# Kernel tuning notes

Hardware: AMD Instinct MI355X
Metric: run time of the kernel (lower is better)

## Reference

```python
import jax, jax.numpy as jnp
import numpy as np

V, ENC, D, E = 10000, 2048, 512, 512
B, L = 128, 64


def setup_inputs() -> dict:
    key = jax.random.key(0)
    ks = jax.random.split(key, 12)
    s = lambda *sh: 1.0 / np.sqrt(sh[-1])
    return {
        "global_feats": jax.random.normal(ks[0], (B, ENC), jnp.float32),
        "encoded_captions": jax.random.randint(ks[1], (B, L), 0, V, jnp.int64),
        "caption_lengths": jax.random.randint(ks[2], (B,), 1, L, jnp.int64),
        "W_embed": jax.random.normal(ks[3], (V, E), jnp.float32) * 0.02,
        "W_init": jax.random.normal(ks[4], (D, ENC), jnp.float32) * s(ENC),
        "b_init": jnp.zeros((D,), jnp.float32),
        "W_ih": jax.random.normal(ks[5], (3 * D, E), jnp.float32) * s(E),
        "W_hh": jax.random.normal(ks[6], (3 * D, D), jnp.float32) * s(D),
        "b_ih": jnp.zeros((3 * D,), jnp.float32),
        "b_hh": jnp.zeros((3 * D,), jnp.float32),
        "W_fc": jax.random.normal(ks[7], (V, D), jnp.float32) * s(D),
        "b_fc": jnp.zeros((V,), jnp.float32),
    }


def reference(global_feats, encoded_captions, caption_lengths,
              W_embed, W_init, b_init, W_ih, W_hh, b_ih, b_hh, W_fc, b_fc):
    # init_hidden: h0 = tanh(Linear(global_feats))  -> (B, D)
    h0 = jnp.tanh(global_feats @ W_init.T + b_init)

    # teacher forcing over timesteps 0..L-2 (PyTorch GRU gate order: r, z, n)
    emb = W_embed[encoded_captions[:, : L - 1]]          # (B, L-1, E)
    gi = jnp.einsum('ble,ge->blg', emb, W_ih) + b_ih     # (B, L-1, 3D) precomputed input gates
    gi = jnp.swapaxes(gi, 0, 1)                          # (L-1, B, 3D) scan over time

    def step(h, gi_t):
        gh = h @ W_hh.T + b_hh                           # (B, 3D)
        i_r, i_z, i_n = jnp.split(gi_t, 3, axis=-1)
        h_r, h_z, h_n = jnp.split(gh, 3, axis=-1)
        r = jax.nn.sigmoid(i_r + h_r)
        z = jax.nn.sigmoid(i_z + h_z)
        n = jnp.tanh(i_n + r * h_n)
        h_new = (1.0 - z) * n + z * h
        return h_new, h_new

    _, hs = jax.lax.scan(step, h0, gi)                   # hs: (L-1, B, D)
    # dropout is identity in eval/reference mode
    logits = jnp.einsum('lbd,vd->blv', hs, W_fc) + b_fc  # (B, L-1, V)
    return logits, caption_lengths - 1
```

## Files before the change

### kernel.cpp

```cpp
#include <hip/hip_runtime.h>
#include <hip/hip_bf16.h>

#define V_    10000
#define ENC_  2048
#define D_    512
#define B_    128
#define L_    64
#define T_    63
#define M_    (B_ * L_ - B_)
#define G_    (3 * D_)
#define LOGITS_SZ ((long)M_ * V_)
#define SCAN_NB 64

typedef __bf16 bf16x8_t __attribute__((ext_vector_type(8)));
typedef float  f32x4_t  __attribute__((ext_vector_type(4)));
typedef short  s16x8_t  __attribute__((ext_vector_type(8)));

typedef __attribute__((address_space(3))) char*       lds_cptr_t;
typedef const __attribute__((address_space(1))) char* glb_cptr_t;

__device__ __forceinline__ void gload_lds16(const void* g, void* l) {
  __builtin_amdgcn_global_load_lds((glb_cptr_t)g, (lds_cptr_t)l, 16, 0, 0);
}
__device__ __forceinline__ float bf2f(short s) {
  return __uint_as_float(((unsigned)(unsigned short)s) << 16);
}
__device__ __forceinline__ short f2bf(float f) {
  __hip_bfloat16 h = __float2bfloat16(f);
  return *reinterpret_cast<short*>(&h);
}
__device__ __forceinline__ s16x8_t cvt8(const float* p) {
  f32x4_t lo = *reinterpret_cast<const f32x4_t*>(p);
  f32x4_t hi = *reinterpret_cast<const f32x4_t*>(p + 4);
  s16x8_t r;
#pragma unroll
  for (int e = 0; e < 4; e++) { r[e] = f2bf(lo[e]); r[4 + e] = f2bf(hi[e]); }
  return r;
}
__device__ __forceinline__ float sigmoidf_(float x) {
  return 1.0f / (1.0f + __expf(-x));
}
__device__ __forceinline__ bf16x8_t lds_frag(const short* p) {
  return __builtin_bit_cast(bf16x8_t, *reinterpret_cast<const s16x8_t*>(p));
}

__global__ void GG_cvt_kernel(const float* __restrict__ src,
                              __hip_bfloat16* __restrict__ dst, int n8) {
  int i = blockIdx.x * blockDim.x + threadIdx.x;
  if (i < n8) {
    s16x8_t v = cvt8(src + (long)i * 8);
    *reinterpret_cast<s16x8_t*>(dst + (long)i * 8) = v;
  }
}

__global__ __launch_bounds__(256) void GG_gemm_h0(
    const __hip_bfloat16* __restrict__ gfB,
    const __hip_bfloat16* __restrict__ WinitB,
    const float* __restrict__ binit,
    __hip_bfloat16* __restrict__ hfull) {
  __shared__ short sA[128 * 64];
  __shared__ short sB[128 * 64];
  const int lane = threadIdx.x & 63;
  const int wave = threadIdx.x >> 6;
  const int n0 = blockIdx.x * 128;
  const int srow = lane >> 3;
  const int scol = (lane & 7) * 8;

  f32x4_t acc[4][4] = {};

  const __hip_bfloat16* aptr[4];
  const __hip_bfloat16* bptr[4];
#pragma unroll
  for (int i = 0; i < 4; i++) {
    const int r = (wave * 4 + i) * 8 + srow;
    aptr[i] = gfB + (long)r * ENC_ + scol;
    bptr[i] = WinitB + (long)(n0 + r) * ENC_ + scol;
  }

  const int wm = (wave >> 1) * 64;
  const int wn = (wave & 1) * 64;
  const int fr = lane & 15;
  const int fk = (lane >> 4) * 8;

  for (int kt = 0; kt < 32; kt++) {
    __syncthreads();
#pragma unroll
    for (int i = 0; i < 4; i++) {
      const int chunk = wave * 4 + i;
      gload_lds16(aptr[i] + kt * 64, sA + chunk * 512);
      gload_lds16(bptr[i] + kt * 64, sB + chunk * 512);
    }
    __syncthreads();
#pragma unroll
    for (int kk = 0; kk < 2; kk++) {
      bf16x8_t a[4], b[4];
#pragma unroll
      for (int i = 0; i < 4; i++) {
        a[i] = lds_frag(sA + (wm + i * 16 + fr) * 64 + kk * 32 + fk);
        b[i] = lds_frag(sB + (wn + i * 16 + fr) * 64 + kk * 32 + fk);
      }
#pragma unroll
      for (int i = 0; i < 4; i++)
#pragma unroll
        for (int j = 0; j < 4; j++)
          acc[i][j] = __builtin_amdgcn_mfma_f32_16x16x32_bf16(a[i], b[j], acc[i][j], 0, 0, 0);
    }
  }

  const int fq = lane >> 4;
#pragma unroll
  for (int j = 0; j < 4; j++) {
    const int n = n0 + wn + j * 16 + fr;
    const float bv = binit[n];
#pragma unroll
    for (int i = 0; i < 4; i++)
#pragma unroll
      for (int rr = 0; rr < 4; rr++) {
        const int m = wm + i * 16 + fq * 4 + rr;
        hfull[(long)m * 64 * 512 + n] = __float2bfloat16(tanhf(acc[i][j][rr] + bv));
      }
  }
}

__global__ __launch_bounds__(256) void GG_gemm_gi(
    const __hip_bfloat16* __restrict__ WembB,
    const int* __restrict__ cap,
    const __hip_bfloat16* __restrict__ WihB,
    const float* __restrict__ bias,
    __hip_bfloat16* __restrict__ C) {
  __shared__ short sA[128 * 64];
  __shared__ short sB[128 * 64];
  const int lane = threadIdx.x & 63;
  const int wave = threadIdx.x >> 6;
  const int m0 = blockIdx.y * 128;
  const int n0 = blockIdx.x * 128;
  const int srow = lane >> 3;
  const int scol = (lane & 7) * 8;

  f32x4_t acc[4][4] = {};

  const __hip_bfloat16* aptr[4];
  const __hip_bfloat16* bptr[4];
#pragma unroll
  for (int i = 0; i < 4; i++) {
    const int r = (wave * 4 + i) * 8 + srow;
    const int bt = m0 + r;
    const int bb = bt / 63;
    const int tt = bt - bb * 63;
    aptr[i] = WembB + (long)cap[bb * L_ + tt] * 512 + scol;
    bptr[i] = WihB + (long)(n0 + r) * 512 + scol;
  }

  const int wm = (wave >> 1) * 64;
  const int wn = (wave & 1) * 64;
  const int fr = lane & 15;
  const int fk = (lane >> 4) * 8;

  for (int kt = 0; kt < 8; kt++) {
    __syncthreads();
#pragma unroll
    for (int i = 0; i < 4; i++) {
      const int chunk = wave * 4 + i;
      gload_lds16(aptr[i] + kt * 64, sA + chunk * 512);
      gload_lds16(bptr[i] + kt * 64, sB + chunk * 512);
    }
    __syncthreads();
#pragma unroll
    for (int kk = 0; kk < 2; kk++) {
      bf16x8_t a[4], b[4];
#pragma unroll
      for (int i = 0; i < 4; i++) {
        a[i] = lds_frag(sA + (wm + i * 16 + fr) * 64 + kk * 32 + fk);
        b[i] = lds_frag(sB + (wn + i * 16 + fr) * 64 + kk * 32 + fk);
      }
#pragma unroll
      for (int i = 0; i < 4; i++)
#pragma unroll
        for (int j = 0; j < 4; j++)
          acc[i][j] = __builtin_amdgcn_mfma_f32_16x16x32_bf16(a[i], b[j], acc[i][j], 0, 0, 0);
    }
  }

  const int fq = lane >> 4;
#pragma unroll
  for (int j = 0; j < 4; j++) {
    const int n = n0 + wn + j * 16 + fr;
    const float bv = bias[n];
#pragma unroll
    for (int i = 0; i < 4; i++)
#pragma unroll
      for (int rr = 0; rr < 4; rr++) {
        const int m = m0 + wm + i * 16 + fq * 4 + rr;
        C[(long)m * G_ + n] = __float2bfloat16(acc[i][j][rr] + bv);
      }
  }
}

template <bool BBF16>
__global__ __launch_bounds__(256) void GG_gemm_logits(
    const __hip_bfloat16* __restrict__ hfull,
    const void* __restrict__ Bsrc,
    const float* __restrict__ bias,
    float* __restrict__ C) {
  const int flat = blockIdx.x;
  const int xcd = flat & 7;
  const int s = flat >> 3;
  const int col = xcd * 10 + s % 10;
  const int row = s / 10;
  if (col >= 79) return;
  const int m0 = row * 128;
  const int n0 = col * 128;

  __shared__ short sA[128 * 64];
  __shared__ short sB[128 * 64];
  const int lane = threadIdx.x & 63;
  const int wave = threadIdx.x >> 6;
  const int srow = lane >> 3;
  const int scol = (lane & 7) * 8;

  f32x4_t acc[4][4] = {};

  const __hip_bfloat16* aptr[4];
  const __hip_bfloat16* bptrB[4];
  const float* bptrF[4];
#pragma unroll
  for (int i = 0; i < 4; i++) {
    const int r = (wave * 4 + i) * 8 + srow;
    const int m = m0 + r;
    const int bb = m / 63;
    const int tt = m - bb * 63;
    aptr[i] = hfull + ((long)bb * 64 + tt + 1) * 512 + scol;
    int nrow = n0 + r;
    nrow = (nrow < V_) ? nrow : (V_ - 1);
    if constexpr (BBF16) bptrB[i] = (const __hip_bfloat16*)Bsrc + (long)nrow * 512 + scol;
    else                 bptrF[i] = (const float*)Bsrc + (long)nrow * 512 + scol;
  }

  const int wm = (wave >> 1) * 64;
  const int wn = (wave & 1) * 64;
  const int fr = lane & 15;
  const int fk = (lane >> 4) * 8;

  for (int kt = 0; kt < 8; kt++) {
    s16x8_t vb[4];
    if constexpr (!BBF16) {
#pragma unroll
      for (int i = 0; i < 4; i++) vb[i] = cvt8(bptrF[i] + kt * 64);
    }
    __syncthreads();
#pragma unroll
    for (int i = 0; i < 4; i++) {
      const int chunk = wave * 4 + i;
      gload_lds16(aptr[i] + kt * 64, sA + chunk * 512);
      if constexpr (BBF16)
        gload_lds16(bptrB[i] + kt * 64, sB + chunk * 512);
      else
        *reinterpret_cast<s16x8_t*>(sB + chunk * 512 + lane * 8) = vb[i];
    }
    __syncthreads();
#pragma unroll
    for (int kk = 0; kk < 2; kk++) {
      bf16x8_t a[4], b[4];
#pragma unroll
      for (int i = 0; i < 4; i++) {
        a[i] = lds_frag(sA + (wm + i * 16 + fr) * 64 + kk * 32 + fk);
        b[i] = lds_frag(sB + (wn + i * 16 + fr) * 64 + kk * 32 + fk);
      }
#pragma unroll
      for (int i = 0; i < 4; i++)
#pragma unroll
        for (int j = 0; j < 4; j++)
          acc[i][j] = __builtin_amdgcn_mfma_f32_16x16x32_bf16(a[i], b[j], acc[i][j], 0, 0, 0);
    }
  }

  const int fq = lane >> 4;
#pragma unroll
  for (int j = 0; j < 4; j++) {
    const int n = n0 + wn + j * 16 + fr;
    if (n >= V_) continue;
    const float bv = bias[n];
#pragma unroll
    for (int i = 0; i < 4; i++)
#pragma unroll
      for (int rr = 0; rr < 4; rr++) {
        const int m = m0 + wm + i * 16 + fq * 4 + rr;
        C[(long)m * V_ + n] = acc[i][j][rr] + bv;
      }
  }
}

__global__ __launch_bounds__(256) void GG_scan_persist(
    __hip_bfloat16* __restrict__ hfull,
    const __hip_bfloat16* __restrict__ gi,
    const __hip_bfloat16* __restrict__ WhhB,
    const float* __restrict__ bhh,
    int* __restrict__ ctr) {
  __shared__ short sW[48 * 512];
  __shared__ short sA[4][16 * 512];
  const int lane = threadIdx.x & 63;
  const int wave = threadIdx.x >> 6;
  const int strip = blockIdx.x & 31;
  const int half  = blockIdx.x >> 5;
  const int d0 = strip * 16;
  const int fr = lane & 15;
  const int g4 = lane >> 4;
  int* myctr = ctr + half * 32;

  for (int rr = wave; rr < 48; rr += 4) {
    const int grow = (rr >> 4) * 512 + d0 + (rr & 15);
    gload_lds16(WhhB + (long)grow * 512 + (lane ^ (rr & 7)) * 8, sW + rr * 512);
  }

  const int dd = d0 + fr;
  const int bbase = half * 64 + wave * 16 + g4 * 4;
  const float br_ = bhh[dd], bz_ = bhh[512 + dd], bn_ = bhh[1024 + dd];
  const short* gis = (const short*)gi;
  short* sAw = &sA[wave][0];

  float hp[4];
#pragma unroll
  for (int rr = 0; rr < 4; rr++)
    hp[rr] = bf2f(*(const short*)&hfull[((long)(bbase + rr) * 64) * 512 + dd]);

  asm volatile("s_waitcnt vmcnt(0)" ::: "memory");
  __syncthreads();

  for (int t = 0; t < T_; t++) {
    short gir[4], giz[4], gin[4];
#pragma unroll
    for (int rr = 0; rr < 4; rr++) {
      const long gbase = ((long)(bbase + rr) * T_ + t) * (long)G_;
      gir[rr] = gis[gbase + dd];
      giz[rr] = gis[gbase + 512 + dd];
      gin[rr] = gis[gbase + 1024 + dd];
    }

    if (t > 0) {
      if (threadIdx.x == 0) {
        while (__hip_atomic_load(myctr, __ATOMIC_ACQUIRE, __HIP_MEMORY_SCOPE_AGENT) <
               t * 32)
          __builtin_amdgcn_s_sleep(1);
      }
      __syncthreads();
    }

#pragma unroll
    for (int r = 0; r < 16; r++) {
      const int b = half * 64 + wave * 16 + r;
      gload_lds16(hfull + ((long)b * 64 + t) * 512 + (lane ^ (r & 7)) * 8,
                  sAw + r * 512);
    }
    asm volatile("s_waitcnt vmcnt(0)" ::: "memory");
    __builtin_amdgcn_sched_barrier(0);

    f32x4_t acc[3] = {};
#pragma unroll
    for (int kt = 0; kt < 8; kt++)
#pragma unroll
      for (int kk = 0; kk < 2; kk++) {
        const int kg = kt * 8 + kk * 4 + g4;
        const int gsw = (kg ^ (fr & 7)) * 8;
        bf16x8_t afr = lds_frag(sAw + fr * 512 + gsw);
        bf16x8_t bfr[3];
#pragma unroll
        for (int j = 0; j < 3; j++) bfr[j] = lds_frag(sW + (j * 16 + fr) * 512 + gsw);
#pragma unroll
        for (int j = 0; j < 3; j++)
          acc[j] = __builtin_amdgcn_mfma_f32_16x16x32_bf16(afr, bfr[j], acc[j], 0, 0, 0);
      }

#pragma unroll
    for (int rr = 0; rr < 4; rr++) {
      const float rg = sigmoidf_(bf2f(gir[rr]) + acc[0][rr] + br_);
      const float zg = sigmoidf_(bf2f(giz[rr]) + acc[1][rr] + bz_);
      const float ng = tanhf(bf2f(gin[rr]) + rg * (acc[2][rr] + bn_));
      const short hnb = f2bf((1.f - zg) * ng + zg * hp[rr]);
      hp[rr] = bf2f(hnb);
      *(short*)&hfull[((long)(bbase + rr) * 64 + t + 1) * 512 + dd] = hnb;
    }

    if (t < T_ - 1) {
      __syncthreads();
      if (threadIdx.x == 0)
        __hip_atomic_fetch_add(myctr, 1, __ATOMIC_RELEASE, __HIP_MEMORY_SCOPE_AGENT);
    }
  }
}

__global__ void GG_tail_kernel(const int* __restrict__ lens, float* __restrict__ out) {
  const int b = threadIdx.x;
  if (b < B_) out[LOGITS_SZ + b] = (float)(lens[b] - 1);
}

extern "C" void kernel_launch(void* const* d_in, const int* in_sizes, int n_in,
                              void* d_out, int out_size, void* d_ws, size_t ws_size,
                              hipStream_t stream) {
  const float* gf      = (const float*)d_in[0];
  const int*   cap     = (const int*)d_in[1];
  const int*   lens    = (const int*)d_in[2];
  const float* W_embed = (const float*)d_in[3];
  const float* W_init  = (const float*)d_in[4];
  const float* b_init  = (const float*)d_in[5];
  const float* W_ih    = (const float*)d_in[6];
  const float* W_hh    = (const float*)d_in[7];
  const float* b_ih    = (const float*)d_in[8];
  const float* b_hh    = (const float*)d_in[9];
  const float* W_fc    = (const float*)d_in[10];
  const float* b_fc    = (const float*)d_in[11];
  float* out = (float*)d_out;

  char* ob = (char*)d_out;
  __hip_bfloat16* gi_ws  = (__hip_bfloat16*)ob;
  __hip_bfloat16* WhhB   = (__hip_bfloat16*)(ob + 25165824);
  __hip_bfloat16* WihB   = (__hip_bfloat16*)(ob + 27262976);
  __hip_bfloat16* WembB  = (__hip_bfloat16*)(ob + 29360128);
  __hip_bfloat16* WinitB = (__hip_bfloat16*)(ob + 40894464);
  __hip_bfloat16* gfB    = (__hip_bfloat16*)(ob + 43253760);

  __hip_bfloat16* hfull = (__hip_bfloat16*)d_ws;
  __hip_bfloat16* WfcB  = (__hip_bfloat16*)((char*)d_ws + 8388608);
  const bool big_ws = ws_size >= (size_t)(8388608 + 10240000 + 256);
  int* ctr = (int*)((char*)d_ws + (big_ws ? 18628608 : 8388608));

  hipMemsetAsync(ctr, 0, 256, stream);

  GG_cvt_kernel<<<dim3((G_ * D_ / 8 + 255) / 256), 256, 0, stream>>>(W_hh, WhhB, G_ * D_ / 8);
  GG_cvt_kernel<<<dim3((G_ * D_ / 8 + 255) / 256), 256, 0, stream>>>(W_ih, WihB, G_ * D_ / 8);
  GG_cvt_kernel<<<dim3((V_ * D_ / 8 + 255) / 256), 256, 0, stream>>>(W_embed, WembB, V_ * D_ / 8);
  GG_cvt_kernel<<<dim3((D_ * ENC_ / 8 + 255) / 256), 256, 0, stream>>>(W_init, WinitB, D_ * ENC_ / 8);
  GG_cvt_kernel<<<dim3((B_ * ENC_ / 8 + 255) / 256), 256, 0, stream>>>(gf, gfB, B_ * ENC_ / 8);
  if (big_ws)
    GG_cvt_kernel<<<dim3((V_ * D_ / 8 + 255) / 256), 256, 0, stream>>>(W_fc, WfcB, V_ * D_ / 8);

  GG_gemm_h0<<<dim3(4), 256, 0, stream>>>(gfB, WinitB, b_init, hfull);

  GG_gemm_gi<<<dim3(G_ / 128, M_ / 128), 256, 0, stream>>>(WembB, cap, WihB, b_ih, gi_ws);

  GG_scan_persist<<<dim3(SCAN_NB), 256, 0, stream>>>(hfull, gi_ws, WhhB, b_hh, ctr);

  if (big_ws)
    GG_gemm_logits<true><<<dim3(5040), 256, 0, stream>>>(hfull, WfcB, b_fc, out);
  else
    GG_gemm_logits<false><<<dim3(5040), 256, 0, stream>>>(hfull, W_fc, b_fc, out);

  GG_tail_kernel<<<dim3(1), 128, 0, stream>>>(lens, out);
}
```

Before: 613.6 us.

## Replace scan atomic counter with per-block flags and fuse weight conversions

The persistent GRU scan now signals step completion by having each block store its step number into its own flag, instead of incrementing a shared atomic counter. Waiters poll all 32 flags at once with one wave and a wave vote. Separately, five fp32-to-bf16 conversion launches are merged into one kernel that picks its source by global index. The goal is to cut contention on the single counter and to remove launch overhead, at the cost of a wider polling read and a hard-coded index partition.

Measured after the change: 590.0 us. -3.8%, faster.

```diff
diff --git a/kernel.cpp b/kernel.cpp
--- a/kernel.cpp
+++ b/kernel.cpp
@@ -42,6 +42,22 @@
 }
 __device__ __forceinline__ bf16x8_t lds_frag(const short* p) {
   return __builtin_bit_cast(bf16x8_t, *reinterpret_cast<const s16x8_t*>(p));
+}
+
+__global__ void GG_cvt5(const float* __restrict__ whh, __hip_bfloat16* __restrict__ dwhh,
+                        const float* __restrict__ wih, __hip_bfloat16* __restrict__ dwih,
+                        const float* __restrict__ wemb, __hip_bfloat16* __restrict__ dwemb,
+                        const float* __restrict__ winit, __hip_bfloat16* __restrict__ dwinit,
+                        const float* __restrict__ gf, __hip_bfloat16* __restrict__ dgf) {
+  const int i = blockIdx.x * blockDim.x + threadIdx.x;
+  const float* s; __hip_bfloat16* d; int off;
+  if (i < 98304)        { s = whh;   d = dwhh;   off = i; }
+  else if (i < 196608)  { s = wih;   d = dwih;   off = i - 98304; }
+  else if (i < 836608)  { s = wemb;  d = dwemb;  off = i - 196608; }
+  else if (i < 967680)  { s = winit; d = dwinit; off = i - 836608; }
+  else                  { s = gf;    d = dgf;    off = i - 967680; }
+  s16x8_t v = cvt8(s + (long)off * 8);
+  *reinterpret_cast<s16x8_t*>(d + (long)off * 8) = v;
 }
 
 __global__ void GG_cvt_kernel(const float* __restrict__ src,
@@ -295,7 +311,7 @@
     const __hip_bfloat16* __restrict__ gi,
     const __hip_bfloat16* __restrict__ WhhB,
     const float* __restrict__ bhh,
-    int* __restrict__ ctr) {
+    int* __restrict__ flagbase) {
   __shared__ short sW[48 * 512];
   __shared__ short sA[4][16 * 512];
   const int lane = threadIdx.x & 63;
@@ -305,7 +321,7 @@
   const int d0 = strip * 16;
   const int fr = lane & 15;
   const int g4 = lane >> 4;
-  int* myctr = ctr + half * 32;
+  int* myflags = flagbase + half * 32;
 
   for (int rr = wave; rr < 48; rr += 4) {
     const int grow = (rr >> 4) * 512 + d0 + (rr & 15);
@@ -337,10 +353,15 @@
     }
 
     if (t > 0) {
-      if (threadIdx.x == 0) {
-        while (__hip_atomic_load(myctr, __ATOMIC_ACQUIRE, __HIP_MEMORY_SCOPE_AGENT) <
-               t * 32)
-          __builtin_amdgcn_s_sleep(1);
+      if (threadIdx.x < 64) {
+        while (true) {
+          int v = t;
+          if (lane < 32)
+            v = __hip_atomic_load(&myflags[lane], __ATOMIC_ACQUIRE,
+                                  __HIP_MEMORY_SCOPE_AGENT);
+          if (__all(v >= t)) break;
+          __builtin_amdgcn_s_sleep(4);
+        }
       }
       __syncthreads();
     }
@@ -383,7 +404,8 @@
     if (t < T_ - 1) {
       __syncthreads();
       if (threadIdx.x == 0)
-        __hip_atomic_fetch_add(myctr, 1, __ATOMIC_RELEASE, __HIP_MEMORY_SCOPE_AGENT);
+        __hip_atomic_store(&myflags[strip], t + 1, __ATOMIC_RELEASE,
+                           __HIP_MEMORY_SCOPE_AGENT);
     }
   }
 }
@@ -421,15 +443,12 @@
   __hip_bfloat16* hfull = (__hip_bfloat16*)d_ws;
   __hip_bfloat16* WfcB  = (__hip_bfloat16*)((char*)d_ws + 8388608);
   const bool big_ws = ws_size >= (size_t)(8388608 + 10240000 + 256);
-  int* ctr = (int*)((char*)d_ws + (big_ws ? 18628608 : 8388608));
-
-  hipMemsetAsync(ctr, 0, 256, stream);
-
-  GG_cvt_kernel<<<dim3((G_ * D_ / 8 + 255) / 256), 256, 0, stream>>>(W_hh, WhhB, G_ * D_ / 8);
-  GG_cvt_kernel<<<dim3((G_ * D_ / 8 + 255) / 256), 256, 0, stream>>>(W_ih, WihB, G_ * D_ / 8);
-  GG_cvt_kernel<<<dim3((V_ * D_ / 8 + 255) / 256), 256, 0, stream>>>(W_embed, WembB, V_ * D_ / 8);
-  GG_cvt_kernel<<<dim3((D_ * ENC_ / 8 + 255) / 256), 256, 0, stream>>>(W_init, WinitB, D_ * ENC_ / 8);
-  GG_cvt_kernel<<<dim3((B_ * ENC_ / 8 + 255) / 256), 256, 0, stream>>>(gf, gfB, B_ * ENC_ / 8);
+  int* flags = (int*)((char*)d_ws + (big_ws ? 18628608 : 8388608));
+
+  hipMemsetAsync(flags, 0, 256, stream);
+
+  GG_cvt5<<<dim3(3908), 256, 0, stream>>>(W_hh, WhhB, W_ih, WihB, W_embed, WembB,
+                                          W_init, WinitB, gf, gfB);
   if (big_ws)
     GG_cvt_kernel<<<dim3((V_ * D_ / 8 + 255) / 256), 256, 0, stream>>>(W_fc, WfcB, V_ * D_ / 8);
 
@@ -437,7 +456,7 @@
 
   GG_gemm_gi<<<dim3(G_ / 128, M_ / 128), 256, 0, stream>>>(WembB, cap, WihB, b_ih, gi_ws);
 
-  GG_scan_persist<<<dim3(SCAN_NB), 256, 0, stream>>>(hfull, gi_ws, WhhB, b_hh, ctr);
+  GG_scan_persist<<<dim3(SCAN_NB), 256, 0, stream>>>(hfull, gi_ws, WhhB, b_hh, flags);
 
   if (big_ws)
     GG_gemm_logits<true><<<dim3(5040), 256, 0, stream>>>(hfull, WfcB, b_fc, out);
```
